# Kernel optimization log

Measured on AMD Instinct MI355X. Metric: run time of the kernel, lower is better.

## Reference

```python
import jax, jax.numpy as jnp
import numpy as np

TOPK = 4

def setup_inputs() -> dict:
    key = jax.random.key(0)
    k1, k2, k3 = jax.random.split(key, 3)
    B, K, C, L = 8, 8, 256, 4096
    xs = jax.random.normal(k1, (B, K, C, L), dtype=jnp.float32)
    # scores are assumed softmax-normalized routing scores in the original
    logits = jax.random.normal(k2, (B, K), dtype=jnp.float32)
    scores = jax.nn.softmax(logits, axis=-1)
    expert_w = jax.random.normal(k3, (K, C, C), dtype=jnp.float32) * 0.02
    expert_b = jnp.zeros((K, C), dtype=jnp.float32)
    return {"xs": xs, "scores": scores, "expert_w": expert_w, "expert_b": expert_b}

def reference(xs, scores, expert_w, expert_b):
    B, K, C, L = xs.shape
    # HardTopKRouting: hard top-k selection, weights renormalized.
    # Backward of the routing is STE returning zero grad to scores.
    tw, sel = jax.lax.top_k(jax.lax.stop_gradient(scores), TOPK)  # [B, topk]
    tw = tw / (tw.sum(axis=-1, keepdims=True) + 1e-8)
    # Dense per-(sample, expert) combine weight; zero for unselected experts.
    w_full = jnp.zeros((B, K), dtype=xs.dtype).at[
        jnp.arange(B)[:, None], sel
    ].set(tw)  # [B, K]
    # Per-expert module (stand-in for Mamba): channel-mixing linear on C.
    # y[b,k,d,l] = sum_c expert_w[k,d,c] * xs[b,k,c,l] + expert_b[k,d]
    y = jnp.einsum('bkcl,kdc->bkdl', xs, expert_w) + expert_b[None, :, :, None]
    # Weighted scatter-add combine: unselected experts have weight 0,
    # matching the original's sparse dispatch/combine math exactly.
    out = jnp.einsum('bk,bkdl->bdl', w_full, y)  # [B, C, L]
    return out
```

## Files before the change

### kernel.cpp

```cpp
#include <hip/hip_runtime.h>

#define B_ 8
#define K_ 8
#define C_ 256
#define L_ 4096
#define TOPK_ 4
#define BN 128
#define BK 32
#define LDST 40

typedef __attribute__((ext_vector_type(8))) short bf16x8;
typedef __attribute__((ext_vector_type(4))) float f32x4;

union P8 { bf16x8 v; unsigned short s[8]; };
union F4 { float4 v; float f[4]; };

__device__ __forceinline__ unsigned short f2bf(float x) {
  unsigned u = __float_as_uint(x);
  u += 0x7fffu + ((u >> 16) & 1u);
  return (unsigned short)(u >> 16);
}

__device__ __forceinline__ void route_b(const float* __restrict__ scores, int b,
                                        float w[TOPK_], int kk[TOPK_]) {
  float s[K_];
#pragma unroll
  for (int k = 0; k < K_; ++k) s[k] = scores[b * K_ + k];
  float sum = 0.f;
#pragma unroll
  for (int i = 0; i < TOPK_; ++i) {
    float bv = -1e30f; int bk = 0;
#pragma unroll
    for (int k = 0; k < K_; ++k)
      if (s[k] > bv) { bv = s[k]; bk = k; }
    kk[i] = bk; w[i] = bv; sum += bv;
    s[bk] = -1e30f;
  }
  float inv = 1.f / (sum + 1e-8f);
#pragma unroll
  for (int i = 0; i < TOPK_; ++i) w[i] *= inv;
}

__global__ __launch_bounds__(256)
void prep_kernel(const float* __restrict__ scores, const float* __restrict__ ew,
                 const float* __restrict__ eb, int* __restrict__ sel,
                 float* __restrict__ biasc, unsigned short* __restrict__ ewb) {
  const int blk = blockIdx.x;
  const int b = blk >> 2, i = blk & 3;
  const int t = threadIdx.x;
  float w[TOPK_]; int kk[TOPK_];
  route_b(scores, b, w, kk);
  if (i == 0) {
    if (t < TOPK_) sel[b * TOPK_ + t] = kk[t];
    float a = 0.f;
#pragma unroll
    for (int j = 0; j < TOPK_; ++j) a += w[j] * eb[kk[j] * C_ + t];
    biasc[b * C_ + t] = a;
  }
  const float wi = w[i];
  const float* src = ew + (size_t)kk[i] * C_ * C_;
  unsigned short* dst = ewb + (size_t)blk * (C_ * C_);
  for (int j = 0; j < 32; ++j) {
    int m = t + 256 * j;
    int d = (m >> 2) & 255;
    int cb = m >> 10;
    int ci = (m & 3) * 8;
    const float* sp = src + d * C_ + cb * 32 + ci;
    F4 a0, a1; a0.v = *(const float4*)sp; a1.v = *(const float4*)(sp + 4);
    P8 p;
#pragma unroll
    for (int e = 0; e < 4; ++e) { p.s[e] = f2bf(wi * a0.f[e]); p.s[4 + e] = f2bf(wi * a1.f[e]); }
    *(bf16x8*)(dst + (size_t)m * 8) = p.v;
  }
}

__global__ __launch_bounds__(256, 1)
void moe_main(const float* __restrict__ xs, const unsigned short* __restrict__ ewb,
              const float* __restrict__ biasc, const int* __restrict__ sel,
              float* __restrict__ out) {
  __shared__ alignas(16) unsigned short As[2][C_ * LDST];
  __shared__ alignas(16) unsigned short Bs[2][BN * LDST];

  const int t = threadIdx.x;
  const int b = blockIdx.y;
  const int l0 = blockIdx.x * BN;
  const int wave = t >> 6;
  const int lane = t & 63;
  const int l16 = lane & 15;
  const int quad = lane >> 4;
  const int lq = (t & 31) * 4;
  const int cq = (t >> 5) * 4;

  int k_s[TOPK_];
#pragma unroll
  for (int i = 0; i < TOPK_; ++i) k_s[i] = sel[b * TOPK_ + i];

  f32x4 acc[4][8];
#pragma unroll
  for (int mi = 0; mi < 4; ++mi)
#pragma unroll
    for (int ni = 0; ni < 8; ++ni)
      acc[mi][ni] = (f32x4){0.f, 0.f, 0.f, 0.f};

  const unsigned short* ewb_b = ewb + (size_t)b * TOPK_ * (C_ * C_);

  bf16x8 ar[4]; F4 br[4];
  auto issue = [&](int s) {
    const int slot = s >> 3, cb = s & 7;
    const unsigned short* ap = ewb_b + (size_t)slot * (C_ * C_) + cb * 8192 + t * 32;
#pragma unroll
    for (int j = 0; j < 4; ++j) ar[j] = *(const bf16x8*)(ap + j * 8);
    const float* xp = xs + (((size_t)b * K_ + k_s[slot]) * C_ + (size_t)(cb * 32 + cq)) * L_ + l0 + lq;
#pragma unroll
    for (int j = 0; j < 4; ++j) br[j].v = *(const float4*)(xp + (size_t)j * L_);
  };

  issue(0);
  for (int s = 0; s < 32; ++s) {
    const int buf = s & 1;
    {
      unsigned short* arow = As[buf] + t * LDST;
#pragma unroll
      for (int j = 0; j < 4; ++j) *(bf16x8*)(arow + j * 8) = ar[j];
#pragma unroll
      for (int i2 = 0; i2 < 4; ++i2) {
        union { unsigned short s4[4]; unsigned long long u; } p;
#pragma unroll
        for (int j = 0; j < 4; ++j) p.s4[j] = f2bf(br[j].f[i2]);
        *(unsigned long long*)(Bs[buf] + (size_t)(lq + i2) * LDST + cq) = p.u;
      }
    }
    if (s + 1 < 32) issue(s + 1);
    __syncthreads();

    bf16x8 af[4], bfr[8];
#pragma unroll
    for (int mi = 0; mi < 4; ++mi)
      af[mi] = *(const bf16x8*)(As[buf] + (size_t)(wave * 64 + mi * 16 + l16) * LDST + quad * 8);
#pragma unroll
    for (int ni = 0; ni < 8; ++ni)
      bfr[ni] = *(const bf16x8*)(Bs[buf] + (size_t)(ni * 16 + l16) * LDST + quad * 8);
#pragma unroll
    for (int mi = 0; mi < 4; ++mi)
#pragma unroll
      for (int ni = 0; ni < 8; ++ni)
        acc[mi][ni] = __builtin_amdgcn_mfma_f32_16x16x32_bf16(af[mi], bfr[ni], acc[mi][ni], 0, 0, 0);
  }

  const float* bc = biasc + b * C_;
#pragma unroll
  for (int mi = 0; mi < 4; ++mi) {
#pragma unroll
    for (int r = 0; r < 4; ++r) {
      const int d = wave * 64 + mi * 16 + quad * 4 + r;
      const float bias = bc[d];
      float* orow = out + ((size_t)b * C_ + d) * L_ + l0;
#pragma unroll
      for (int ni = 0; ni < 8; ++ni)
        orow[ni * 16 + l16] = acc[mi][ni][r] + bias;
    }
  }
}

extern "C" void kernel_launch(void* const* d_in, const int* in_sizes, int n_in,
                              void* d_out, int out_size, void* d_ws, size_t ws_size,
                              hipStream_t stream) {
  const float* xs     = (const float*)d_in[0];
  const float* scores = (const float*)d_in[1];
  const float* ew     = (const float*)d_in[2];
  const float* eb     = (const float*)d_in[3];
  float* out = (float*)d_out;

  int*   sel   = (int*)d_ws;
  float* biasc = (float*)((char*)d_ws + 1024);
  unsigned short* ewb = (unsigned short*)((char*)d_ws + 16384);

  prep_kernel<<<B_ * TOPK_, 256, 0, stream>>>(scores, ew, eb, sel, biasc, ewb);
  dim3 grid(L_ / BN, B_);
  moe_main<<<grid, 256, 0, stream>>>(xs, ewb, biasc, sel, out);
}
```

Measured before the change: 348.5 us.

## Pre-swizzle expert weights into MFMA fragment layout and bypass LDS for A

The prep kernel now writes the scaled bf16 expert weights directly in the per-lane MFMA A-fragment order, so the main kernel loads A fragments straight from global memory into registers and drops the A shared-memory tile. The loop is fully unrolled with double-buffered register prefetch, the next-stage prefetch is moved after the barrier, and the xs-to-LDS transpose mapping is changed and uses packed bf16 conversion intrinsics. The goal is to cut LDS traffic and shared memory use. The cost is higher register pressure from the doubled prefetch buffers and the full unroll, which may hurt occupancy or cause spills.

```diff
diff --git a/kernel.cpp b/kernel.cpp
--- a/kernel.cpp
+++ b/kernel.cpp
@@ -1,4 +1,5 @@
 #include <hip/hip_runtime.h>
+#include <hip/hip_bf16.h>
 
 #define B_ 8
 #define K_ 8
@@ -6,13 +7,11 @@
 #define L_ 4096
 #define TOPK_ 4
 #define BN 128
-#define BK 32
 #define LDST 40
 
 typedef __attribute__((ext_vector_type(8))) short bf16x8;
 typedef __attribute__((ext_vector_type(4))) float f32x4;
 
-union P8 { bf16x8 v; unsigned short s[8]; };
 union F4 { float4 v; float f[4]; };
 
 __device__ __forceinline__ unsigned short f2bf(float x) {
@@ -59,18 +58,23 @@
   }
   const float wi = w[i];
   const float* src = ew + (size_t)kk[i] * C_ * C_;
-  unsigned short* dst = ewb + (size_t)blk * (C_ * C_);
-  for (int j = 0; j < 32; ++j) {
-    int m = t + 256 * j;
-    int d = (m >> 2) & 255;
-    int cb = m >> 10;
-    int ci = (m & 3) * 8;
-    const float* sp = src + d * C_ + cb * 32 + ci;
-    F4 a0, a1; a0.v = *(const float4*)sp; a1.v = *(const float4*)(sp + 4);
-    P8 p;
+  unsigned short* dst = ewb + (size_t)blk * 65536;
+  const int dlo = t & 15, q = (t >> 4) & 3, wv = t >> 6;
 #pragma unroll
-    for (int e = 0; e < 4; ++e) { p.s[e] = f2bf(wi * a0.f[e]); p.s[4 + e] = f2bf(wi * a1.f[e]); }
-    *(bf16x8*)(dst + (size_t)m * 8) = p.v;
+  for (int cb = 0; cb < 8; ++cb) {
+#pragma unroll
+    for (int mi = 0; mi < 4; ++mi) {
+      const int d = wv * 64 + mi * 16 + dlo;
+      const float* sp = src + d * C_ + cb * 32 + q * 8;
+      F4 a0, a1; a0.v = *(const float4*)sp; a1.v = *(const float4*)(sp + 4);
+      union { unsigned short s[8]; bf16x8 v; } p;
+#pragma unroll
+      for (int e = 0; e < 4; ++e) {
+        p.s[e]     = f2bf(wi * a0.f[e]);
+        p.s[4 + e] = f2bf(wi * a1.f[e]);
+      }
+      *(bf16x8*)(dst + cb * 8192 + (mi * 256 + t) * 8) = p.v;
+    }
   }
 }
 
@@ -78,7 +82,6 @@
 void moe_main(const float* __restrict__ xs, const unsigned short* __restrict__ ewb,
               const float* __restrict__ biasc, const int* __restrict__ sel,
               float* __restrict__ out) {
-  __shared__ alignas(16) unsigned short As[2][C_ * LDST];
   __shared__ alignas(16) unsigned short Bs[2][BN * LDST];
 
   const int t = threadIdx.x;
@@ -88,8 +91,8 @@
   const int lane = t & 63;
   const int l16 = lane & 15;
   const int quad = lane >> 4;
-  const int lq = (t & 31) * 4;
-  const int cq = (t >> 5) * 4;
+  const int cg = t & 7;
+  const int lg = t >> 3;
 
   int k_s[TOPK_];
 #pragma unroll
@@ -102,50 +105,46 @@
     for (int ni = 0; ni < 8; ++ni)
       acc[mi][ni] = (f32x4){0.f, 0.f, 0.f, 0.f};
 
-  const unsigned short* ewb_b = ewb + (size_t)b * TOPK_ * (C_ * C_);
+  const unsigned short* ewb_b = ewb + (size_t)b * TOPK_ * 65536;
+  bf16x8 arbuf[2][4];
+  F4     brbuf[2][4];
 
-  bf16x8 ar[4]; F4 br[4];
-  auto issue = [&](int s) {
-    const int slot = s >> 3, cb = s & 7;
-    const unsigned short* ap = ewb_b + (size_t)slot * (C_ * C_) + cb * 8192 + t * 32;
+#define ISSUE(S) do {                                                         \
+    const int slot_ = (S) >> 3, cb_ = (S) & 7, pb_ = (S) & 1;                 \
+    const unsigned short* ap_ = ewb_b + slot_ * 65536 + cb_ * 8192;           \
+    _Pragma("unroll") for (int mi = 0; mi < 4; ++mi)                          \
+      arbuf[pb_][mi] = *(const bf16x8*)(ap_ + (mi * 256 + t) * 8);            \
+    const float* xp_ = xs + (((size_t)b * K_ + k_s[slot_]) * C_ +             \
+                             (size_t)(cb_ * 32 + cg * 4)) * L_ + l0 + lg * 4; \
+    _Pragma("unroll") for (int j = 0; j < 4; ++j)                             \
+      brbuf[pb_][j].v = *(const float4*)(xp_ + (size_t)j * L_);               \
+  } while (0)
+
+  ISSUE(0);
 #pragma unroll
-    for (int j = 0; j < 4; ++j) ar[j] = *(const bf16x8*)(ap + j * 8);
-    const float* xp = xs + (((size_t)b * K_ + k_s[slot]) * C_ + (size_t)(cb * 32 + cq)) * L_ + l0 + lq;
-#pragma unroll
-    for (int j = 0; j < 4; ++j) br[j].v = *(const float4*)(xp + (size_t)j * L_);
-  };
-
-  issue(0);
   for (int s = 0; s < 32; ++s) {
     const int buf = s & 1;
-    {
-      unsigned short* arow = As[buf] + t * LDST;
+    unsigned short* brow = Bs[buf] + (lg * 4) * LDST + cg * 4;
 #pragma unroll
-      for (int j = 0; j < 4; ++j) *(bf16x8*)(arow + j * 8) = ar[j];
-#pragma unroll
-      for (int i2 = 0; i2 < 4; ++i2) {
-        union { unsigned short s4[4]; unsigned long long u; } p;
-#pragma unroll
-        for (int j = 0; j < 4; ++j) p.s4[j] = f2bf(br[j].f[i2]);
-        *(unsigned long long*)(Bs[buf] + (size_t)(lq + i2) * LDST + cq) = p.u;
-      }
+    for (int i2 = 0; i2 < 4; ++i2) {
+      union { __hip_bfloat162 h[2]; unsigned long long u; } pk;
+      pk.h[0] = __float22bfloat162_rn(make_float2(brbuf[buf][0].f[i2], brbuf[buf][1].f[i2]));
+      pk.h[1] = __float22bfloat162_rn(make_float2(brbuf[buf][2].f[i2], brbuf[buf][3].f[i2]));
+      *(unsigned long long*)(brow + i2 * LDST) = pk.u;
     }
-    if (s + 1 < 32) issue(s + 1);
     __syncthreads();
-
-    bf16x8 af[4], bfr[8];
-#pragma unroll
-    for (int mi = 0; mi < 4; ++mi)
-      af[mi] = *(const bf16x8*)(As[buf] + (size_t)(wave * 64 + mi * 16 + l16) * LDST + quad * 8);
+    if (s + 1 < 32) ISSUE(s + 1);
+    bf16x8 bfr[8];
 #pragma unroll
     for (int ni = 0; ni < 8; ++ni)
-      bfr[ni] = *(const bf16x8*)(Bs[buf] + (size_t)(ni * 16 + l16) * LDST + quad * 8);
+      bfr[ni] = *(const bf16x8*)(Bs[buf] + (ni * 16 + l16) * LDST + quad * 8);
 #pragma unroll
     for (int mi = 0; mi < 4; ++mi)
 #pragma unroll
       for (int ni = 0; ni < 8; ++ni)
-        acc[mi][ni] = __builtin_amdgcn_mfma_f32_16x16x32_bf16(af[mi], bfr[ni], acc[mi][ni], 0, 0, 0);
+        acc[mi][ni] = __builtin_amdgcn_mfma_f32_16x16x32_bf16(arbuf[buf][mi], bfr[ni], acc[mi][ni], 0, 0, 0);
   }
+#undef ISSUE
 
   const float* bc = biasc + b * C_;
 #pragma unroll
```

New measurement: 350.5 us. Within noise of the previous version (+0.6%).
